# Optimization experiments

Measured on AMD Instinct MI355X. Metric: run time of the kernel, lower is better.

## Reference

```python
import jax, jax.numpy as jnp
import numpy as np

C = 512
QK = C // 8  # 64
B, L = 8, 4096


def setup_inputs() -> dict:
    key = jax.random.key(0)
    ks = jax.random.split(key, 8)
    s = 0.02
    return {
        "x": jax.random.normal(ks[0], (B, C, L), dtype=jnp.float32),
        "Wq": jax.random.normal(ks[1], (QK, C), dtype=jnp.float32) * s,
        "bq": jax.random.normal(ks[2], (QK,), dtype=jnp.float32) * s,
        "Wk": jax.random.normal(ks[3], (QK, C), dtype=jnp.float32) * s,
        "bk": jax.random.normal(ks[4], (QK,), dtype=jnp.float32) * s,
        "Wv": jax.random.normal(ks[5], (C, C), dtype=jnp.float32) * s,
        "bv": jax.random.normal(ks[6], (C,), dtype=jnp.float32) * s,
        "gamma": jax.random.normal(ks[7], (1,), dtype=jnp.float32) * 0.1,
    }


def reference(x, Wq, bq, Wk, bk, Wv, bv, gamma):
    # 1x1 convs are per-position linear projections over channels
    q = jnp.einsum('bcl,dc->bld', x, Wq) + bq            # [B, L, QK]  (proj_query, permuted)
    k = jnp.einsum('bcl,dc->bdl', x, Wk) + bk[:, None]   # [B, QK, L]  (proj_key)
    v = jnp.einsum('bcl,dc->bdl', x, Wv) + bv[:, None]   # [B, C, L]   (proj_value)
    energy = jnp.einsum('bid,bdj->bij', q, k)            # [B, L, L]
    attn = jax.nn.softmax(energy, axis=-1)               # softmax over j
    out = jnp.einsum('bcj,bij->bci', v, attn)            # [B, C, L]
    return gamma * out + x
```

## Files before the change

kernel.cpp:

```cpp
#include <hip/hip_runtime.h>
#include <math.h>

#define BB 8
#define CC 512
#define LL 4096
#define DQK 64

typedef short short8 __attribute__((ext_vector_type(8)));
typedef unsigned short ushort4v __attribute__((ext_vector_type(4)));
typedef unsigned short ushort8v __attribute__((ext_vector_type(8)));
typedef float floatx4 __attribute__((ext_vector_type(4)));
typedef unsigned int uint4v __attribute__((ext_vector_type(4)));

__device__ __forceinline__ unsigned short f2bf(float f) {
    union { float f; unsigned u; } v; v.f = f;
    unsigned r = v.u + 0x7fffu + ((v.u >> 16) & 1u);
    return (unsigned short)(r >> 16);
}

__device__ __forceinline__ void load_lds16(const void* gptr, void* lptr) {
    __builtin_amdgcn_global_load_lds(
        (const __attribute__((address_space(1))) unsigned int*)gptr,
        (__attribute__((address_space(3))) unsigned int*)lptr, 16, 0, 0);
}

__device__ __forceinline__ unsigned cvt_pk_bf16(float lo, float hi) {
    unsigned r;
    asm("v_cvt_pk_bf16_f32 %0, %1, %2" : "=v"(r) : "v"(lo), "v"(hi));
    return r;
}

__global__ void k_castw(const float* __restrict__ wq, const float* __restrict__ wk,
                        const float* __restrict__ wv,
                        unsigned short* __restrict__ wqb, unsigned short* __restrict__ wkb,
                        unsigned short* __restrict__ wvb) {
    int i = blockIdx.x * 256 + threadIdx.x;
    if (i < DQK * CC) { wqb[i] = f2bf(wq[i]); wkb[i] = f2bf(wk[i]); }
    wvb[i] = f2bf(wv[i]);
}

__global__ __launch_bounds__(256) void k_prep(const float* __restrict__ x,
                                              const unsigned short* __restrict__ wqb,
                                              const unsigned short* __restrict__ wkb,
                                              const unsigned short* __restrict__ wvb,
                                              const float* __restrict__ bq,
                                              const float* __restrict__ bk,
                                              const float* __restrict__ bv,
                                              unsigned short* __restrict__ qout,
                                              unsigned short* __restrict__ kout,
                                              unsigned short* __restrict__ vout) {
    int l0 = blockIdx.x * 64;
    int b  = blockIdx.y;
    int tid = threadIdx.x;
    int w = tid >> 6, lane = tid & 63;
    int lane16 = lane & 15, g = lane >> 4;
    __shared__ unsigned short xtile[64 * 512];

    {
        int cr = tid >> 2;
        int ch = (tid & 3) * 16;
#pragma unroll
        for (int cc = 0; cc < 8; ++cc) {
            int c  = cc * 64 + cr;
            int gc = c >> 3;
            int cl = c & 7;
            const float* src = x + ((size_t)b * CC + c) * LL + l0 + ch;
#pragma unroll
            for (int j = 0; j < 4; ++j) {
                floatx4 v = *(const floatx4*)(src + j * 4);
#pragma unroll
                for (int e = 0; e < 4; ++e) {
                    int l  = ch + j * 4 + e;
                    int pg = (gc & 56) | ((gc ^ (l & 7)) & 7);
                    xtile[l * 512 + pg * 8 + cl] = f2bf(v[e]);
                }
            }
        }
    }

    int xe = (g ^ (lane16 & 7)) * 8;
    int xo = ((g + 4) ^ (lane16 & 7)) * 8;

    auto loadW8 = [&](short8 (&af)[8], int hs) {
        int z = hs >> 1, kh = hs & 1;
        const unsigned short* base;
        if (z < 8)       base = wvb + (size_t)(z * 64 + w * 16 + lane16) * CC;
        else if (z == 8) base = wqb + (size_t)(w * 16 + lane16) * CC;
        else             base = wkb + (size_t)(w * 16 + lane16) * CC;
        base += g * 8 + kh * 256;
#pragma unroll
        for (int kk = 0; kk < 8; ++kk) af[kk] = *(const short8*)(base + kk * 32);
    };

    short8 wA[8], wB[8];
    loadW8(wA, 0);
    __syncthreads();

    for (int z = 0; z < 10; ++z) {
        loadW8(wB, z * 2 + 1);
        floatx4 acc[4];
#pragma unroll
        for (int nt = 0; nt < 4; ++nt) acc[nt] = {0.f, 0.f, 0.f, 0.f};
#pragma unroll
        for (int nt = 0; nt < 4; ++nt)
#pragma unroll
            for (int kk = 0; kk < 8; ++kk) {
                int off = (nt * 16 + lane16) * 512 + (kk >> 1) * 64 + ((kk & 1) ? xo : xe);
                short8 bfrag = *(const short8*)(xtile + off);
                acc[nt] = __builtin_amdgcn_mfma_f32_16x16x32_bf16(wA[kk], bfrag, acc[nt], 0, 0, 0);
            }
        if (z + 1 < 10) loadW8(wA, (z + 1) * 2);
#pragma unroll
        for (int nt = 0; nt < 4; ++nt)
#pragma unroll
            for (int kk = 0; kk < 8; ++kk) {
                int kk8 = kk + 8;
                int off = (nt * 16 + lane16) * 512 + (kk8 >> 1) * 64 + ((kk8 & 1) ? xo : xe);
                short8 bfrag = *(const short8*)(xtile + off);
                acc[nt] = __builtin_amdgcn_mfma_f32_16x16x32_bf16(wB[kk], bfrag, acc[nt], 0, 0, 0);
            }
#pragma unroll
        for (int nt = 0; nt < 4; ++nt) {
            int l = l0 + nt * 16 + lane16;
            if (z < 8) {
#pragma unroll
                for (int r = 0; r < 4; ++r) {
                    int d = z * 64 + w * 16 + g * 4 + r;
                    vout[((size_t)b * CC + d) * LL + l] = f2bf(acc[nt][r] + bv[d]);
                }
            } else {
                const float* bias = (z == 8) ? bq : bk;
                float sc = (z == 8) ? 1.4426950408889634f : 1.0f;
                ushort4v o;
#pragma unroll
                for (int r = 0; r < 4; ++r)
                    o[r] = f2bf((acc[nt][r] + bias[w * 16 + g * 4 + r]) * sc);
                unsigned short* dst = ((z == 8) ? qout : kout)
                                      + ((size_t)b * LL + l) * DQK + w * 16 + g * 4;
                *(ushort4v*)dst = o;
            }
        }
    }
}

__global__ __launch_bounds__(256, 2) void k_attn(const unsigned short* __restrict__ q,
                                                 const unsigned short* __restrict__ kws,
                                                 const unsigned short* __restrict__ vws,
                                                 const float* __restrict__ x,
                                                 const float* __restrict__ gamma,
                                                 float* __restrict__ out) {
    int bid = blockIdx.x + 32 * blockIdx.y + 256 * blockIdx.z;
    int x8  = bid & 7;
    int ii  = bid >> 3;
    int wg  = (x8 + 8 * (ii >> 5)) * 32 + (ii & 31);
    int i0 = (wg & 31) * 128;
    int b  = (wg >> 5) & 7;
    int c0 = (wg >> 8) * 256;

    int tid = threadIdx.x;
    int w = tid >> 6, lane = tid & 63;
    int lane16 = lane & 15, g = lane >> 4;
    int iw = i0 + w * 32;

    __shared__ unsigned short kt[2][64 * 64];
    __shared__ unsigned short vt[2][256 * 64];

    short8 qf[2][2];
#pragma unroll
    for (int m = 0; m < 2; ++m) {
        const unsigned short* qrow = q + ((size_t)b * LL + iw + m * 16 + lane16) * DQK + g * 8;
        qf[m][0] = *(const short8*)(qrow);
        qf[m][1] = *(const short8*)(qrow + 32);
    }

    const unsigned short* kglob = kws + (size_t)b * LL * DQK;
    const unsigned short* vglob = vws + ((size_t)b * CC + c0) * LL;
    int gr    = (tid & 7) ^ ((tid >> 3) & 7);
    int koff0 = (tid >> 3) * DQK + gr * 8;
    int voff0 = (tid >> 3) * LL  + gr * 8;

    int kro[2], vro[2];
#pragma unroll
    for (int kk = 0; kk < 2; ++kk) {
        int sw = (kk * 4 + g) ^ (lane16 & 7);
        kro[kk] = lane16 * 64 + sw * 8;
        vro[kk] = lane16 * 64 + sw * 8;
    }

    short8 ones;
#pragma unroll
    for (int j = 0; j < 8; ++j) ones[j] = (short)0x3f80;

    floatx4 O[2][16];
#pragma unroll
    for (int m = 0; m < 2; ++m)
#pragma unroll
        for (int nt = 0; nt < 16; ++nt) O[m][nt] = {0.f, 0.f, 0.f, 0.f};
    floatx4 Ol[2];
#pragma unroll
    for (int m = 0; m < 2; ++m) Ol[m] = {0.f, 0.f, 0.f, 0.f};

    auto stage = [&](int j0n, int buf) {
        const unsigned short* ks = kglob + j0n * DQK + koff0;
        unsigned short* kd = &kt[buf][tid * 8];
        load_lds16(ks,        kd);
        load_lds16(ks + 2048, kd + 2048);
        const unsigned short* vs = vglob + j0n + voff0;
        unsigned short* vd = &vt[buf][tid * 8];
#pragma unroll
        for (int i = 0; i < 8; ++i)
            load_lds16(vs + i * 131072, vd + i * 2048);
    };

    auto softmax_half = [&](floatx4 (&Sh)[2][2], short8 (&paD)[2]) {
#pragma unroll
        for (int m = 0; m < 2; ++m) {
            float e0[4], e1[4];
#pragma unroll
            for (int r = 0; r < 4; ++r) {
                e0[r] = __builtin_amdgcn_exp2f(Sh[m][0][r]);
                e1[r] = __builtin_amdgcn_exp2f(Sh[m][1][r]);
            }
            unsigned A0 = cvt_pk_bf16(e0[0], e0[1]);
            unsigned A1 = cvt_pk_bf16(e0[2], e0[3]);
            unsigned B0 = cvt_pk_bf16(e1[0], e1[1]);
            unsigned B1 = cvt_pk_bf16(e1[2], e1[3]);
            asm("v_permlane32_swap_b32 %0, %1" : "+v"(A0), "+v"(B0));
            asm("v_permlane16_swap_b32 %0, %1" : "+v"(A0), "+v"(B0));
            asm("v_permlane32_swap_b32 %0, %1" : "+v"(A1), "+v"(B1));
            asm("v_permlane16_swap_b32 %0, %1" : "+v"(A1), "+v"(B1));
            uint4v pw = { A0, A1, B0, B1 };
            paD[m] = *(short8*)&pw;
            Ol[m] = __builtin_amdgcn_mfma_f32_16x16x32_bf16(paD[m], ones, Ol[m], 0, 0, 0);
        }
    };

    stage(0, 0);
    int cur = 0;
    for (int j0 = 0; j0 < LL; j0 += 64) {
        __syncthreads();
        if (j0 + 64 < LL) stage(j0 + 64, cur ^ 1);

        const unsigned short* kbp = kt[cur];
        const unsigned short* vbp = vt[cur];

        floatx4 Sa[2][2], Sb[2][2];
#pragma unroll
        for (int m = 0; m < 2; ++m)
#pragma unroll
            for (int nt = 0; nt < 2; ++nt) { Sa[m][nt] = {0.f,0.f,0.f,0.f}; Sb[m][nt] = {0.f,0.f,0.f,0.f}; }

        short8 ka0 = *(const short8*)(kbp + kro[0]);
        short8 ka1 = *(const short8*)(kbp + kro[1]);
        short8 kb0 = *(const short8*)(kbp + kro[0] + 1024);
        short8 kb1 = *(const short8*)(kbp + kro[1] + 1024);
#pragma unroll
        for (int m = 0; m < 2; ++m) {
            Sa[m][0] = __builtin_amdgcn_mfma_f32_16x16x32_bf16(ka0, qf[m][0], Sa[m][0], 0, 0, 0);
            Sa[m][0] = __builtin_amdgcn_mfma_f32_16x16x32_bf16(ka1, qf[m][1], Sa[m][0], 0, 0, 0);
            Sa[m][1] = __builtin_amdgcn_mfma_f32_16x16x32_bf16(kb0, qf[m][0], Sa[m][1], 0, 0, 0);
            Sa[m][1] = __builtin_amdgcn_mfma_f32_16x16x32_bf16(kb1, qf[m][1], Sa[m][1], 0, 0, 0);
        }
        short8 kc0 = *(const short8*)(kbp + kro[0] + 2048);
        short8 kc1 = *(const short8*)(kbp + kro[1] + 2048);
        short8 kd0 = *(const short8*)(kbp + kro[0] + 3072);
        short8 kd1 = *(const short8*)(kbp + kro[1] + 3072);
#pragma unroll
        for (int m = 0; m < 2; ++m) {
            Sb[m][0] = __builtin_amdgcn_mfma_f32_16x16x32_bf16(kc0, qf[m][0], Sb[m][0], 0, 0, 0);
            Sb[m][0] = __builtin_amdgcn_mfma_f32_16x16x32_bf16(kc1, qf[m][1], Sb[m][0], 0, 0, 0);
            Sb[m][1] = __builtin_amdgcn_mfma_f32_16x16x32_bf16(kd0, qf[m][0], Sb[m][1], 0, 0, 0);
            Sb[m][1] = __builtin_amdgcn_mfma_f32_16x16x32_bf16(kd1, qf[m][1], Sb[m][1], 0, 0, 0);
        }

        short8 pa0[2], pa1[2];
        softmax_half(Sa, pa0);

        __builtin_amdgcn_s_setprio(1);
#pragma unroll
        for (int nt = 0; nt < 8; ++nt) {
            short8 vf = *(const short8*)(vbp + vro[0] + nt * 1024);
#pragma unroll
            for (int m = 0; m < 2; ++m)
                O[m][nt] = __builtin_amdgcn_mfma_f32_16x16x32_bf16(pa0[m], vf, O[m][nt], 0, 0, 0);
        }
        __builtin_amdgcn_s_setprio(0);

        softmax_half(Sb, pa1);

        __builtin_amdgcn_s_setprio(1);
#pragma unroll
        for (int nt = 8; nt < 16; ++nt) {
            short8 vf = *(const short8*)(vbp + vro[0] + nt * 1024);
#pragma unroll
            for (int m = 0; m < 2; ++m)
                O[m][nt] = __builtin_amdgcn_mfma_f32_16x16x32_bf16(pa0[m], vf, O[m][nt], 0, 0, 0);
        }
#pragma unroll
        for (int nt = 0; nt < 16; ++nt) {
            short8 vf = *(const short8*)(vbp + vro[1] + nt * 1024);
#pragma unroll
            for (int m = 0; m < 2; ++m)
                O[m][nt] = __builtin_amdgcn_mfma_f32_16x16x32_bf16(pa1[m], vf, O[m][nt], 0, 0, 0);
        }
        __builtin_amdgcn_s_setprio(0);
        cur ^= 1;
    }

    float linv[2][4];
#pragma unroll
    for (int m = 0; m < 2; ++m)
#pragma unroll
        for (int r = 0; r < 4; ++r) linv[m][r] = 1.f / Ol[m][r];

    float gam = gamma[0];
#pragma unroll
    for (int m = 0; m < 2; ++m)
#pragma unroll
        for (int nt = 0; nt < 16; ++nt) {
            int c = c0 + nt * 16 + lane16;
            size_t base = ((size_t)b * CC + c) * LL + iw + m * 16 + g * 4;
            floatx4 xv = *(const floatx4*)(x + base);
            floatx4 o;
#pragma unroll
            for (int r = 0; r < 4; ++r) o[r] = gam * (O[m][nt][r] * linv[m][r]) + xv[r];
            *(floatx4*)(out + base) = o;
        }
}

extern "C" void kernel_launch(void* const* d_in, const int* in_sizes, int n_in,
                              void* d_out, int out_size, void* d_ws, size_t ws_size,
                              hipStream_t stream) {
    const float* x     = (const float*)d_in[0];
    const float* Wq    = (const float*)d_in[1];
    const float* bq    = (const float*)d_in[2];
    const float* Wk    = (const float*)d_in[3];
    const float* bk    = (const float*)d_in[4];
    const float* Wv    = (const float*)d_in[5];
    const float* bv    = (const float*)d_in[6];
    const float* gamma = (const float*)d_in[7];
    float* out = (float*)d_out;

    unsigned short* qb  = (unsigned short*)d_ws;
    unsigned short* kb  = qb  + (size_t)BB * LL * DQK;
    unsigned short* vb  = kb  + (size_t)BB * LL * DQK;
    unsigned short* wqb = vb  + (size_t)BB * CC * LL;
    unsigned short* wkb = wqb + (size_t)DQK * CC;
    unsigned short* wvb = wkb + (size_t)DQK * CC;

    k_castw<<<dim3((CC * CC) / 256), 256, 0, stream>>>(Wq, Wk, Wv, wqb, wkb, wvb);
    k_prep<<<dim3(LL / 64, BB), 256, 0, stream>>>(x, wqb, wkb, wvb, bq, bk, bv, qb, kb, vb);
    k_attn<<<dim3(LL / 128, BB, CC / 256), 256, 0, stream>>>(qb, kb, vb, x, gamma, out);
}
```

Measured before the change: 339.7 us.

## Coalesce V stores through LDS staging and pipeline x tile loads in prep

The prep kernel now loads x as float2 per lane across eight channels with double-buffered register prefetch, packs them with v_cvt_pk_bf16 and writes 16-byte vectors into the swizzled LDS tile. Before, each thread issued scalar 2-byte LDS writes. The V projection swaps the MFMA operand order so each lane holds contiguous positions, then stages the bf16 results in a per-wave LDS buffer and writes V rows with 16-byte coalesced global stores. This replaces the old strided 2-byte scattered stores. Q and K projections move to a separate loop. The cost is extra LDS space plus explicit waitcnt and sched barriers.

```diff
diff --git a/kernel.cpp b/kernel.cpp
--- a/kernel.cpp
+++ b/kernel.cpp
@@ -10,6 +10,7 @@
 typedef unsigned short ushort4v __attribute__((ext_vector_type(4)));
 typedef unsigned short ushort8v __attribute__((ext_vector_type(8)));
 typedef float floatx4 __attribute__((ext_vector_type(4)));
+typedef float floatx2 __attribute__((ext_vector_type(2)));
 typedef unsigned int uint4v __attribute__((ext_vector_type(4)));
 
 __device__ __forceinline__ unsigned short f2bf(float f) {
@@ -55,26 +56,39 @@
     int w = tid >> 6, lane = tid & 63;
     int lane16 = lane & 15, g = lane >> 4;
     __shared__ unsigned short xtile[64 * 512];
+    __shared__ unsigned short wstage[4][16 * 72];
 
     {
-        int cr = tid >> 2;
-        int ch = (tid & 3) * 16;
-#pragma unroll
-        for (int cc = 0; cc < 8; ++cc) {
-            int c  = cc * 64 + cr;
-            int gc = c >> 3;
-            int cl = c & 7;
-            const float* src = x + ((size_t)b * CC + c) * LL + l0 + ch;
-#pragma unroll
-            for (int j = 0; j < 4; ++j) {
-                floatx4 v = *(const floatx4*)(src + j * 4);
-#pragma unroll
-                for (int e = 0; e < 4; ++e) {
-                    int l  = ch + j * 4 + e;
-                    int pg = (gc & 56) | ((gc ^ (l & 7)) & 7);
-                    xtile[l * 512 + pg * 8 + cl] = f2bf(v[e]);
-                }
-            }
+        int cset = w * 2 + (lane >> 5);
+        int lp   = lane & 31;
+        const float* xb = x + ((size_t)b * CC + cset * 64) * LL + l0 + 2 * lp;
+
+        floatx2 ld0[8], ld1[8];
+        auto ldg = [&](floatx2* dst, int gj) {
+#pragma unroll
+            for (int k = 0; k < 8; ++k)
+                dst[k] = *(const floatx2*)(xb + (size_t)(gj * 8 + k) * LL);
+        };
+        auto wr = [&](floatx2* src, int gj) {
+            int cg = cset * 8 + gj;
+#pragma unroll
+            for (int e = 0; e < 2; ++e) {
+                int l  = 2 * lp + e;
+                int pg = (cg & 56) | ((cg ^ (l & 7)) & 7);
+                uint4v u = { cvt_pk_bf16(src[0][e], src[1][e]),
+                             cvt_pk_bf16(src[2][e], src[3][e]),
+                             cvt_pk_bf16(src[4][e], src[5][e]),
+                             cvt_pk_bf16(src[6][e], src[7][e]) };
+                *(uint4v*)(xtile + l * 512 + pg * 8) = u;
+            }
+        };
+        ldg(ld0, 0);
+        ldg(ld1, 1);
+#pragma unroll
+        for (int gj = 0; gj < 8; ++gj) {
+            floatx2* cur = (gj & 1) ? ld1 : ld0;
+            wr(cur, gj);
+            if (gj + 2 < 8) ldg(cur, gj + 2);
         }
     }
 
@@ -96,7 +110,50 @@
     loadW8(wA, 0);
     __syncthreads();
 
-    for (int z = 0; z < 10; ++z) {
+    unsigned short* ws = &wstage[w][0];
+    for (int z = 0; z < 8; ++z) {
+        loadW8(wB, z * 2 + 1);
+        floatx4 acc[4];
+#pragma unroll
+        for (int nt = 0; nt < 4; ++nt) acc[nt] = {0.f, 0.f, 0.f, 0.f};
+#pragma unroll
+        for (int nt = 0; nt < 4; ++nt)
+#pragma unroll
+            for (int kk = 0; kk < 8; ++kk) {
+                int off = (nt * 16 + lane16) * 512 + (kk >> 1) * 64 + ((kk & 1) ? xo : xe);
+                short8 bfrag = *(const short8*)(xtile + off);
+                acc[nt] = __builtin_amdgcn_mfma_f32_16x16x32_bf16(bfrag, wA[kk], acc[nt], 0, 0, 0);
+            }
+        loadW8(wA, (z + 1) * 2);
+#pragma unroll
+        for (int nt = 0; nt < 4; ++nt)
+#pragma unroll
+            for (int kk = 0; kk < 8; ++kk) {
+                int kk8 = kk + 8;
+                int off = (nt * 16 + lane16) * 512 + (kk8 >> 1) * 64 + ((kk8 & 1) ? xo : xe);
+                short8 bfrag = *(const short8*)(xtile + off);
+                acc[nt] = __builtin_amdgcn_mfma_f32_16x16x32_bf16(bfrag, wB[kk], acc[nt], 0, 0, 0);
+            }
+        float bd = bv[z * 64 + w * 16 + lane16];
+#pragma unroll
+        for (int nt = 0; nt < 4; ++nt) {
+            ushort4v o = { f2bf(acc[nt][0] + bd), f2bf(acc[nt][1] + bd),
+                           f2bf(acc[nt][2] + bd), f2bf(acc[nt][3] + bd) };
+            *(ushort4v*)(ws + lane16 * 72 + nt * 16 + g * 4) = o;
+        }
+        asm volatile("s_waitcnt lgkmcnt(0)" ::: "memory");
+        __builtin_amdgcn_sched_barrier(0);
+        int dr = lane >> 2, lc = lane & 3;
+        ushort8v r0 = *(const ushort8v*)(ws + dr * 72 + lc * 16);
+        ushort8v r1 = *(const ushort8v*)(ws + dr * 72 + lc * 16 + 8);
+        size_t vbase = ((size_t)b * CC + z * 64 + w * 16 + dr) * LL + l0 + lc * 16;
+        *(ushort8v*)(vout + vbase)     = r0;
+        *(ushort8v*)(vout + vbase + 8) = r1;
+        asm volatile("s_waitcnt lgkmcnt(0)" ::: "memory");
+        __builtin_amdgcn_sched_barrier(0);
+    }
+
+    for (int z = 8; z < 10; ++z) {
         loadW8(wB, z * 2 + 1);
         floatx4 acc[4];
 #pragma unroll
@@ -119,26 +176,18 @@
                 short8 bfrag = *(const short8*)(xtile + off);
                 acc[nt] = __builtin_amdgcn_mfma_f32_16x16x32_bf16(wB[kk], bfrag, acc[nt], 0, 0, 0);
             }
+        const float* bias = (z == 8) ? bq : bk;
+        float sc = (z == 8) ? 1.4426950408889634f : 1.0f;
 #pragma unroll
         for (int nt = 0; nt < 4; ++nt) {
             int l = l0 + nt * 16 + lane16;
-            if (z < 8) {
-#pragma unroll
-                for (int r = 0; r < 4; ++r) {
-                    int d = z * 64 + w * 16 + g * 4 + r;
-                    vout[((size_t)b * CC + d) * LL + l] = f2bf(acc[nt][r] + bv[d]);
-                }
-            } else {
-                const float* bias = (z == 8) ? bq : bk;
-                float sc = (z == 8) ? 1.4426950408889634f : 1.0f;
-                ushort4v o;
-#pragma unroll
-                for (int r = 0; r < 4; ++r)
-                    o[r] = f2bf((acc[nt][r] + bias[w * 16 + g * 4 + r]) * sc);
-                unsigned short* dst = ((z == 8) ? qout : kout)
-                                      + ((size_t)b * LL + l) * DQK + w * 16 + g * 4;
-                *(ushort4v*)dst = o;
-            }
+            ushort4v o;
+#pragma unroll
+            for (int r = 0; r < 4; ++r)
+                o[r] = f2bf((acc[nt][r] + bias[w * 16 + g * 4 + r]) * sc);
+            unsigned short* dst = ((z == 8) ? qout : kout)
+                                  + ((size_t)b * LL + l) * DQK + w * 16 + g * 4;
+            *(ushort4v*)dst = o;
         }
     }
 }
```

Measured after the change: 329.0 us. -3.1%, faster.

## Restructure QKV projection kernel with 32-position tiles and 32x32 MFMA

Applied to the files above, without the earlier changes.

The projection kernel now handles 32 sequence positions per block instead of 64, doubling the grid. It uses 32x32x16 bf16 MFMA tiles with two interleaved accumulators and double-buffered weight fragments in place of 16x16x32 tiles. The x tile is loaded as float2 pairs and packed to bf16 with v_cvt_pk_bf16 into 16-byte LDS stores. The aim is more parallelism and fewer LDS and convert instructions, at the cost of re-reading the weights for twice as many blocks and more strided scalar output stores.

```diff
diff --git a/kernel.cpp b/kernel.cpp
--- a/kernel.cpp
+++ b/kernel.cpp
@@ -10,6 +10,8 @@
 typedef unsigned short ushort4v __attribute__((ext_vector_type(4)));
 typedef unsigned short ushort8v __attribute__((ext_vector_type(8)));
 typedef float floatx4 __attribute__((ext_vector_type(4)));
+typedef float floatx2 __attribute__((ext_vector_type(2)));
+typedef float floatx16 __attribute__((ext_vector_type(16)));
 typedef unsigned int uint4v __attribute__((ext_vector_type(4)));
 
 __device__ __forceinline__ unsigned short f2bf(float f) {
@@ -49,95 +51,101 @@
                                               unsigned short* __restrict__ qout,
                                               unsigned short* __restrict__ kout,
                                               unsigned short* __restrict__ vout) {
-    int l0 = blockIdx.x * 64;
+    int l0 = blockIdx.x * 32;
     int b  = blockIdx.y;
     int tid = threadIdx.x;
     int w = tid >> 6, lane = tid & 63;
-    int lane16 = lane & 15, g = lane >> 4;
-    __shared__ unsigned short xtile[64 * 512];
+    int l32 = lane & 31, lh = lane >> 5;
+    __shared__ unsigned short xtile[32 * 512];
 
     {
-        int cr = tid >> 2;
-        int ch = (tid & 3) * 16;
-#pragma unroll
-        for (int cc = 0; cc < 8; ++cc) {
-            int c  = cc * 64 + cr;
-            int gc = c >> 3;
-            int cl = c & 7;
-            const float* src = x + ((size_t)b * CC + c) * LL + l0 + ch;
-#pragma unroll
-            for (int j = 0; j < 4; ++j) {
-                floatx4 v = *(const floatx4*)(src + j * 4);
-#pragma unroll
-                for (int e = 0; e < 4; ++e) {
-                    int l  = ch + j * 4 + e;
-                    int pg = (gc & 56) | ((gc ^ (l & 7)) & 7);
-                    xtile[l * 512 + pg * 8 + cl] = f2bf(v[e]);
+        int cset = tid >> 4;
+        int lp   = tid & 15;
+        const float* xb = x + ((size_t)b * CC + cset * 32) * LL + l0 + 2 * lp;
+        floatx2 A[8], B[8];
+        auto ldg8 = [&](floatx2* d, int cg) {
+#pragma unroll
+            for (int k = 0; k < 8; ++k) d[k] = *(const floatx2*)(xb + (size_t)(cg * 8 + k) * LL);
+        };
+        auto wr8 = [&](floatx2* s, int cg) {
+            int gi = cset * 4 + cg;
+#pragma unroll
+            for (int e = 0; e < 2; ++e) {
+                int l  = 2 * lp + e;
+                int pg = (gi & 56) | ((gi ^ (l & 7)) & 7);
+                uint4v u = { cvt_pk_bf16(s[0][e], s[1][e]), cvt_pk_bf16(s[2][e], s[3][e]),
+                             cvt_pk_bf16(s[4][e], s[5][e]), cvt_pk_bf16(s[6][e], s[7][e]) };
+                *(uint4v*)(xtile + l * 512 + pg * 8) = u;
+            }
+        };
+        ldg8(A, 0); ldg8(B, 1);
+        wr8(A, 0);  ldg8(A, 2);
+        wr8(B, 1);  ldg8(B, 3);
+        wr8(A, 2);  wr8(B, 3);
+    }
+    __syncthreads();
+
+    const unsigned short* xbase[4];
+#pragma unroll
+    for (int j = 0; j < 4; ++j) {
+        int low = (((j * 2 + lh) ^ (l32 & 7)) & 7) * 8;
+        xbase[j] = xtile + l32 * 512 + low;
+    }
+
+    for (int step = 0; step < 5; ++step) {
+        bool isV = (step < 4);
+        int dbase = isV ? (step * 128 + w * 32) : ((w & 1) * 32);
+        const unsigned short* wsrc = isV ? wvb : ((w >> 1) ? wkb : wqb);
+        const unsigned short* wrow = wsrc + (size_t)(dbase + l32) * CC + lh * 8;
+
+        short8 wfA[8], wfB[8];
+#pragma unroll
+        for (int k = 0; k < 8; ++k) wfA[k] = *(const short8*)(wrow + k * 32);
+
+        floatx16 acc0, acc1;
+#pragma unroll
+        for (int r = 0; r < 16; ++r) { acc0[r] = 0.f; acc1[r] = 0.f; }
+
+#pragma unroll
+        for (int kg = 0; kg < 4; ++kg) {
+            short8* cur = (kg & 1) ? wfB : wfA;
+            short8* nxt = (kg & 1) ? wfA : wfB;
+            if (kg < 3) {
+#pragma unroll
+                for (int k = 0; k < 8; ++k)
+                    nxt[k] = *(const short8*)(wrow + (kg + 1) * 256 + k * 32);
+            }
+#pragma unroll
+            for (int kk = 0; kk < 8; ++kk) {
+                int ks = kg * 8 + kk;
+                short8 xf = *(const short8*)(xbase[ks & 3] + (ks >> 2) * 64);
+                if (isV) {
+                    if (ks & 1) acc1 = __builtin_amdgcn_mfma_f32_32x32x16_bf16(cur[kk], xf, acc1, 0, 0, 0);
+                    else        acc0 = __builtin_amdgcn_mfma_f32_32x32x16_bf16(cur[kk], xf, acc0, 0, 0, 0);
+                } else {
+                    if (ks & 1) acc1 = __builtin_amdgcn_mfma_f32_32x32x16_bf16(xf, cur[kk], acc1, 0, 0, 0);
+                    else        acc0 = __builtin_amdgcn_mfma_f32_32x32x16_bf16(xf, cur[kk], acc0, 0, 0, 0);
                 }
             }
         }
-    }
-
-    int xe = (g ^ (lane16 & 7)) * 8;
-    int xo = ((g + 4) ^ (lane16 & 7)) * 8;
-
-    auto loadW8 = [&](short8 (&af)[8], int hs) {
-        int z = hs >> 1, kh = hs & 1;
-        const unsigned short* base;
-        if (z < 8)       base = wvb + (size_t)(z * 64 + w * 16 + lane16) * CC;
-        else if (z == 8) base = wqb + (size_t)(w * 16 + lane16) * CC;
-        else             base = wkb + (size_t)(w * 16 + lane16) * CC;
-        base += g * 8 + kh * 256;
-#pragma unroll
-        for (int kk = 0; kk < 8; ++kk) af[kk] = *(const short8*)(base + kk * 32);
-    };
-
-    short8 wA[8], wB[8];
-    loadW8(wA, 0);
-    __syncthreads();
-
-    for (int z = 0; z < 10; ++z) {
-        loadW8(wB, z * 2 + 1);
-        floatx4 acc[4];
-#pragma unroll
-        for (int nt = 0; nt < 4; ++nt) acc[nt] = {0.f, 0.f, 0.f, 0.f};
-#pragma unroll
-        for (int nt = 0; nt < 4; ++nt)
-#pragma unroll
-            for (int kk = 0; kk < 8; ++kk) {
-                int off = (nt * 16 + lane16) * 512 + (kk >> 1) * 64 + ((kk & 1) ? xo : xe);
-                short8 bfrag = *(const short8*)(xtile + off);
-                acc[nt] = __builtin_amdgcn_mfma_f32_16x16x32_bf16(wA[kk], bfrag, acc[nt], 0, 0, 0);
-            }
-        if (z + 1 < 10) loadW8(wA, (z + 1) * 2);
-#pragma unroll
-        for (int nt = 0; nt < 4; ++nt)
-#pragma unroll
-            for (int kk = 0; kk < 8; ++kk) {
-                int kk8 = kk + 8;
-                int off = (nt * 16 + lane16) * 512 + (kk8 >> 1) * 64 + ((kk8 & 1) ? xo : xe);
-                short8 bfrag = *(const short8*)(xtile + off);
-                acc[nt] = __builtin_amdgcn_mfma_f32_16x16x32_bf16(wB[kk], bfrag, acc[nt], 0, 0, 0);
-            }
-#pragma unroll
-        for (int nt = 0; nt < 4; ++nt) {
-            int l = l0 + nt * 16 + lane16;
-            if (z < 8) {
-#pragma unroll
-                for (int r = 0; r < 4; ++r) {
-                    int d = z * 64 + w * 16 + g * 4 + r;
-                    vout[((size_t)b * CC + d) * LL + l] = f2bf(acc[nt][r] + bv[d]);
-                }
-            } else {
-                const float* bias = (z == 8) ? bq : bk;
-                float sc = (z == 8) ? 1.4426950408889634f : 1.0f;
-                ushort4v o;
-#pragma unroll
-                for (int r = 0; r < 4; ++r)
-                    o[r] = f2bf((acc[nt][r] + bias[w * 16 + g * 4 + r]) * sc);
-                unsigned short* dst = ((z == 8) ? qout : kout)
-                                      + ((size_t)b * LL + l) * DQK + w * 16 + g * 4;
-                *(ushort4v*)dst = o;
+
+        if (isV) {
+#pragma unroll
+            for (int r = 0; r < 16; ++r) {
+                int d = dbase + (r & 3) + 8 * (r >> 2) + 4 * lh;
+                float v = acc0[r] + acc1[r] + bv[d];
+                vout[((size_t)b * CC + d) * LL + l0 + l32] = f2bf(v);
+            }
+        } else {
+            const float* bias = (w >> 1) ? bk : bq;
+            float sc = (w >> 1) ? 1.0f : 1.4426950408889634f;
+            float bd = bias[dbase + l32];
+            unsigned short* dst = ((w >> 1) ? kout : qout) + (size_t)b * LL * DQK + dbase + l32;
+#pragma unroll
+            for (int r = 0; r < 16; ++r) {
+                int l = l0 + (r & 3) + 8 * (r >> 2) + 4 * lh;
+                float v = (acc0[r] + acc1[r] + bd) * sc;
+                dst[(size_t)l * DQK] = f2bf(v);
             }
         }
     }
@@ -349,6 +357,6 @@
     unsigned short* wvb = wkb + (size_t)DQK * CC;
 
     k_castw<<<dim3((CC * CC) / 256), 256, 0, stream>>>(Wq, Wk, Wv, wqb, wkb, wvb);
-    k_prep<<<dim3(LL / 64, BB), 256, 0, stream>>>(x, wqb, wkb, wvb, bq, bk, bv, qb, kb, vb);
+    k_prep<<<dim3(LL / 32, BB), 256, 0, stream>>>(x, wqb, wkb, wvb, bq, bk, bv, qb, kb, vb);
     k_attn<<<dim3(LL / 128, BB, CC / 256), 256, 0, stream>>>(qb, kb, vb, x, gamma, out);
 }
```

New measurement: 353.9 us. 4.2% more time.
